# Kernel tuning notes

Hardware: AMD Instinct MI355X
Metric: run time of the kernel (lower is better)

The kernel has to match this reference:

```python
import jax, jax.numpy as jnp
import numpy as np

D_MODEL = 768
KAN_HIDDEN = 2048
NUM_CP = 16        # number of B-spline control points / coefficients per edge
DEGREE = 3         # cubic splines
RMIN, RMAX = -4.0, 4.0


def bspline_basis(x, num_cp=NUM_CP, degree=DEGREE, rmin=RMIN, rmax=RMAX):
    """Cox-de Boor B-spline basis.
    x: (N, D) -> basis: (N, D, num_cp). Uniform knots extended by `degree`
    on each side so that [rmin, rmax] has full basis support.
    """
    h = (rmax - rmin) / (num_cp - degree)
    # K = num_cp + degree + 1 knots
    knots = rmin - degree * h + jnp.arange(num_cp + degree + 1, dtype=x.dtype) * h
    xe = x[..., None]  # (N, D, 1)
    # degree-0 indicator bases: (N, D, num_cp + degree)
    b = ((xe >= knots[:-1]) & (xe < knots[1:])).astype(x.dtype)
    for d in range(1, degree + 1):
        t0 = knots[:-(d + 1)]   # t[k]
        t1 = knots[d:-1]        # t[k+d]
        t2 = knots[d + 1:]      # t[k+d+1]
        t3 = knots[1:-d]        # t[k+1]
        b = (xe - t0) / (t1 - t0) * b[..., :-1] + (t2 - xe) / (t2 - t3) * b[..., 1:]
    return b  # (N, D, num_cp)


def kan_layer(x, w):
    """x: (N, Din); w: (Dout, Din, num_cp) per-edge spline coefficients."""
    basis = bspline_basis(x)                      # (N, Din, K)
    return jnp.einsum('ndk,odk->no', basis, w)    # (N, Dout)


def setup_inputs() -> dict:
    key = jax.random.key(0)
    kx, k1, k2 = jax.random.split(key, 3)
    x = jax.random.normal(kx, (2, 2048, D_MODEL), dtype=jnp.float32)
    # spline coefficient tables, small init like nn.init scaled normal
    w1 = jax.random.normal(k1, (KAN_HIDDEN, D_MODEL, NUM_CP), dtype=jnp.float32) * (1.0 / np.sqrt(D_MODEL * NUM_CP))
    w2 = jax.random.normal(k2, (D_MODEL, KAN_HIDDEN, NUM_CP), dtype=jnp.float32) * (1.0 / np.sqrt(KAN_HIDDEN * NUM_CP))
    return {"x": x, "w1": w1, "w2": w2}


def reference(x, w1, w2):
    B, T, D = x.shape
    input_dtype = x.dtype
    h = x.reshape(B * T, D).astype(jnp.float32)
    h = kan_layer(h, w1)                # (B*T, KAN_HIDDEN)
    h = kan_layer(h, w2)                # (B*T, D_MODEL)
    h = h.astype(input_dtype)
    # dropout p=0.0 / eval mode -> identity
    return h.reshape(B, T, -1)
```

## Files before the change

### kernel.cpp

```cpp
#include <hip/hip_runtime.h>
#include <hip/hip_bf16.h>
#include <stdint.h>

typedef __attribute__((ext_vector_type(8))) short short8;
typedef __attribute__((ext_vector_type(4))) float f32x4;
typedef __attribute__((ext_vector_type(4))) int i32x4;

#define DMODEL 768
#define HID    2048
#define MROWS  4096

#define KINVH  (13.0f/8.0f)
#define KNOT0  (-4.0f - 3.0f*(8.0f/13.0f))

__device__ __forceinline__ unsigned short f2bf(float f) {
  __hip_bfloat16 h = __float2bfloat16(f);
  return *reinterpret_cast<unsigned short*>(&h);
}

template<int DIN>
__device__ __forceinline__ void pack_wave(const float* __restrict__ src,
                                          unsigned short* __restrict__ dst, int gw) {
  constexpr int NK2 = DIN / 2;
  int l   = threadIdx.x & 63;
  int cb  = gw / NK2;
  int kt2 = gw % NK2;
  int c16 = l & 15, q = l >> 4;
  int col = cb * 16 + c16;
  const float* s = src + ((size_t)col * DIN + kt2 * 2 + (q >> 1)) * 16 + (q & 1) * 8;
  float4 v0 = *(const float4*)s;
  float4 v1 = *(const float4*)(s + 4);
  short8 o;
  o[0] = (short)f2bf(v0.x); o[1] = (short)f2bf(v0.y);
  o[2] = (short)f2bf(v0.z); o[3] = (short)f2bf(v0.w);
  o[4] = (short)f2bf(v1.x); o[5] = (short)f2bf(v1.y);
  o[6] = (short)f2bf(v1.z); o[7] = (short)f2bf(v1.w);
  *(short8*)(dst + (((size_t)cb * NK2 + kt2) * 64 + q * 16 + c16) * 8) = o;
}

__global__ void __launch_bounds__(256) conv_pack1(const float* __restrict__ src,
                                                  unsigned short* __restrict__ dst) {
  pack_wave<DMODEL>(src, dst, blockIdx.x * 4 + (threadIdx.x >> 6));
}

__global__ void __launch_bounds__(256) pack2_reduce2(const float* __restrict__ w2,
                                                     unsigned short* __restrict__ dst,
                                                     float4* __restrict__ p, int n4) {
  constexpr int PACK_BLOCKS = ((DMODEL / 16) * (HID / 2)) / 4;
  int b = blockIdx.x;
  if (b < PACK_BLOCKS) {
    pack_wave<HID>(w2, dst, b * 4 + (threadIdx.x >> 6));
  } else {
    int i = (b - PACK_BLOCKS) * 256 + threadIdx.x;
    if (i < n4) {
      float4 a = p[i], q = p[i + n4];
      float4 r;
      r.x = a.x + q.x; r.y = a.y + q.y; r.z = a.z + q.z; r.w = a.w + q.w;
      p[i] = r;
    }
  }
}

__global__ void __launch_bounds__(256) reduce4(const float4* __restrict__ p,
                                               float4* __restrict__ out, int n4) {
  int i = blockIdx.x * 256 + threadIdx.x;
  if (i >= n4) return;
  float4 a = p[i], b = p[i + n4], c = p[i + 2 * n4], d = p[i + 3 * n4];
  float4 r;
  r.x = a.x + b.x + c.x + d.x;
  r.y = a.y + b.y + c.y + d.y;
  r.z = a.z + b.z + c.z + d.z;
  r.w = a.w + b.w + c.w + d.w;
  out[i] = r;
}

template<int DIN, int DOUT, int SPLITK>
__global__ void __launch_bounds__(256, 4)
kan_gemm(const float* __restrict__ X, const unsigned short* __restrict__ Wb,
         float* __restrict__ Out) {
  constexpr int BM  = 64;
  constexpr int BN  = 256;
  constexpr int NK  = (DIN * 16) / 64;
  constexpr int NK2 = DIN / 2;
  constexpr int NKS = NK / SPLITK;
  constexpr int GX  = MROWS / BM;
  constexpr int GY  = DOUT / BN;
  constexpr int CPX = (GX * GY) / 8;
  __shared__ __align__(16) char smA[BM * 128];

  const int tid  = threadIdx.x;
  const int lane = tid & 63;
  const int wid  = tid >> 6;

  const int d    = blockIdx.x + blockIdx.y * GX;
  const int lf   = (d & 7) * CPX + (d >> 3);
  const int brow = (lf % GX) * BM;
  const int bcol = (lf / GX) * BN;
  const int kt0  = blockIdx.z * NKS;
  const int kt1  = kt0 + NKS;

  f32x4 acc[4][4];
#pragma unroll
  for (int m = 0; m < 4; ++m)
#pragma unroll
    for (int n = 0; n < 4; ++n) acc[m][n] = (f32x4){0.f, 0.f, 0.f, 0.f};

  int a_base[4], a_sw[4];
#pragma unroll
  for (int m = 0; m < 4; ++m) {
    int row   = m * 16 + (lane & 15);
    a_base[m] = row * 128 + ((lane >> 4) * 16);
    a_sw[m]   = (row & 7) << 4;
  }

  const unsigned short* bp[4];
#pragma unroll
  for (int n = 0; n < 4; ++n)
    bp[n] = Wb + ((size_t)(bcol / 16 + wid * 4 + n) * NK2 + (size_t)kt0 * 2) * 512
               + lane * 8;

  const int br_ = tid >> 2;
  const int bd_ = tid & 3;
  const float* xrow = X + (size_t)(brow + br_) * DIN + bd_;

  float xcur = xrow[(size_t)kt0 * 4];
  short8 bv[2][4];
#pragma unroll
  for (int n = 0; n < 4; ++n) {
    bv[0][n] = *(const short8*)(bp[n]);
    bv[1][n] = *(const short8*)(bp[n] + 512);
    bp[n] += 1024;
  }

  for (int kt = kt0; kt < kt1; ++kt) {
    __syncthreads();

    {
      float u  = (xcur - KNOT0) * KINVH;
      float uf = floorf(u);
      int   jj = (int)uf;
      float t  = u - uf;
      float s1 = 1.0f - t;
      float t2 = t * t, t3 = t2 * t;
      float s2 = s1 * s1, s3 = s2 * s1;
      float p0 = s3 * (1.0f / 6.0f);
      float p3 = t3 * (1.0f / 6.0f);
      float p1 = fmaf(0.5f, t3, 2.0f / 3.0f) - t2;
      float p2 = fmaf(0.5f, s3, 2.0f / 3.0f) - s2;

      int base = br_ * 128 + bd_ * 32;
      int sw   = (br_ & 7) << 4;
      *(i32x4*)(smA + (base ^ sw))        = (i32x4){0, 0, 0, 0};
      *(i32x4*)(smA + ((base + 16) ^ sw)) = (i32x4){0, 0, 0, 0};
      unsigned short q0 = f2bf(p0), q1 = f2bf(p1), q2 = f2bf(p2), q3 = f2bf(p3);
      int k0 = jj - 3;
      if ((unsigned)(k0 + 0) < 16u) *(unsigned short*)(smA + ((base + (k0 + 0) * 2) ^ sw)) = q0;
      if ((unsigned)(k0 + 1) < 16u) *(unsigned short*)(smA + ((base + (k0 + 1) * 2) ^ sw)) = q1;
      if ((unsigned)(k0 + 2) < 16u) *(unsigned short*)(smA + ((base + (k0 + 2) * 2) ^ sw)) = q2;
      if ((unsigned)(k0 + 3) < 16u) *(unsigned short*)(smA + ((base + (k0 + 3) * 2) ^ sw)) = q3;
    }

    {
      int ktn = (kt + 1 < kt1) ? kt + 1 : kt;
      xcur = xrow[(size_t)ktn * 4];
    }

    __syncthreads();

#pragma unroll
    for (int kk = 0; kk < 2; ++kk) {
      short8 a[4];
#pragma unroll
      for (int m = 0; m < 4; ++m)
        a[m] = *(const short8*)(smA + ((a_base[m] + kk * 64) ^ a_sw[m]));
#pragma unroll
      for (int m = 0; m < 4; ++m)
#pragma unroll
        for (int n = 0; n < 4; ++n)
          acc[m][n] = __builtin_amdgcn_mfma_f32_16x16x32_bf16(a[m], bv[kk][n], acc[m][n], 0, 0, 0);
    }

    if (kt + 1 < kt1) {
#pragma unroll
      for (int n = 0; n < 4; ++n) {
        bv[0][n] = *(const short8*)(bp[n]);
        bv[1][n] = *(const short8*)(bp[n] + 512);
        bp[n] += 1024;
      }
    }
  }

  float* outp = Out + (size_t)blockIdx.z * MROWS * DOUT;
#pragma unroll
  for (int m = 0; m < 4; ++m)
#pragma unroll
    for (int n = 0; n < 4; ++n)
#pragma unroll
      for (int q = 0; q < 4; ++q) {
        int grow = brow + m * 16 + (lane >> 4) * 4 + q;
        int gcol = bcol + wid * 64 + n * 16 + (lane & 15);
        outp[(size_t)grow * DOUT + gcol] = acc[m][n][q];
      }
}

extern "C" void kernel_launch(void* const* d_in, const int* in_sizes, int n_in,
                              void* d_out, int out_size, void* d_ws, size_t ws_size,
                              hipStream_t stream) {
  const float* x  = (const float*)d_in[0];
  const float* w1 = (const float*)d_in[1];
  const float* w2 = (const float*)d_in[2];
  float* out = (float*)d_out;

  char* ws = (char*)d_ws;
  unsigned short* wgb   = (unsigned short*)ws;
  float*          part1 = (float*)(ws + 50331648);
  float*          hbf   = part1;
  float*          part2 = (float*)(ws + 83886080);

  conv_pack1<<<((HID / 16) * (DMODEL / 2)) / 4, 256, 0, stream>>>(w1, wgb);
  kan_gemm<DMODEL, HID, 2>
      <<<dim3(MROWS / 64, HID / 256, 2), 256, 0, stream>>>(x, wgb, part1);

  {
    const int hn4 = (MROWS * HID) / 4;
    const int packB = ((DMODEL / 16) * (HID / 2)) / 4;
    const int redB  = hn4 / 256;
    pack2_reduce2<<<packB + redB, 256, 0, stream>>>(w2, wgb, (float4*)part1, hn4);
  }
  kan_gemm<HID, DMODEL, 4>
      <<<dim3(MROWS / 64, DMODEL / 256, 4), 256, 0, stream>>>(hbf, wgb, part2);
  const int rn4 = (MROWS * DMODEL) / 4;
  reduce4<<<rn4 / 256, 256, 0, stream>>>((const float4*)part2, (float4*)out, rn4);
}
```

Before: 443.9 us.

## Warp-specialize KAN GEMM into basis-producer and MFMA-consumer waves with double-buffered LDS

Doubles the block to 512 threads. Four producer waves evaluate the B-spline basis into one of two LDS buffers while four consumer waves run MFMAs on the other, with one barrier per K-step instead of two. The aim is to hide the basis computation and LDS writes behind the matrix math. In exchange, each block uses more threads and twice the LDS, which may lower occupancy (launch_bounds 512,4), and producer waves sit idle during the epilogue.

```diff
diff --git a/kernel.cpp b/kernel.cpp
--- a/kernel.cpp
+++ b/kernel.cpp
@@ -12,6 +12,10 @@
 
 #define KINVH  (13.0f/8.0f)
 #define KNOT0  (-4.0f - 3.0f*(8.0f/13.0f))
+
+#define BAR_LDS() do { asm volatile("s_waitcnt lgkmcnt(0)" ::: "memory"); \
+                       __builtin_amdgcn_s_barrier(); \
+                       __builtin_amdgcn_sched_barrier(0); } while (0)
 
 __device__ __forceinline__ unsigned short f2bf(float f) {
   __hip_bfloat16 h = __float2bfloat16(f);
@@ -75,7 +79,7 @@
 }
 
 template<int DIN, int DOUT, int SPLITK>
-__global__ void __launch_bounds__(256, 4)
+__global__ void __launch_bounds__(512, 4)
 kan_gemm(const float* __restrict__ X, const unsigned short* __restrict__ Wb,
          float* __restrict__ Out) {
   constexpr int BM  = 64;
@@ -83,14 +87,17 @@
   constexpr int NK  = (DIN * 16) / 64;
   constexpr int NK2 = DIN / 2;
   constexpr int NKS = NK / SPLITK;
+  static_assert(NKS % 2 == 0, "even K-steps for buffer parity");
   constexpr int GX  = MROWS / BM;
   constexpr int GY  = DOUT / BN;
   constexpr int CPX = (GX * GY) / 8;
-  __shared__ __align__(16) char smA[BM * 128];
+  __shared__ __align__(16) char smA[2][BM * 128];
 
   const int tid  = threadIdx.x;
   const int lane = tid & 63;
   const int wid  = tid >> 6;
+  const bool prod = (wid >= 4);
+  const int cwid = wid & 3;
 
   const int d    = blockIdx.x + blockIdx.y * GX;
   const int lf   = (d & 7) * CPX + (d >> 3);
@@ -112,84 +119,96 @@
     a_base[m] = row * 128 + ((lane >> 4) * 16);
     a_sw[m]   = (row & 7) << 4;
   }
-
   const unsigned short* bp[4];
 #pragma unroll
   for (int n = 0; n < 4; ++n)
-    bp[n] = Wb + ((size_t)(bcol / 16 + wid * 4 + n) * NK2 + (size_t)kt0 * 2) * 512
+    bp[n] = Wb + ((size_t)(bcol / 16 + cwid * 4 + n) * NK2 + (size_t)kt0 * 2) * 512
                + lane * 8;
-
-  const int br_ = tid >> 2;
-  const int bd_ = tid & 3;
+  short8 bv[2][4];
+
+  const int pt  = tid & 255;
+  const int br_ = pt >> 2;
+  const int bd_ = pt & 3;
   const float* xrow = X + (size_t)(brow + br_) * DIN + bd_;
-
-  float xcur = xrow[(size_t)kt0 * 4];
-  short8 bv[2][4];
-#pragma unroll
-  for (int n = 0; n < 4; ++n) {
-    bv[0][n] = *(const short8*)(bp[n]);
-    bv[1][n] = *(const short8*)(bp[n] + 512);
-    bp[n] += 1024;
-  }
-
-  for (int kt = kt0; kt < kt1; ++kt) {
-    __syncthreads();
-
-    {
-      float u  = (xcur - KNOT0) * KINVH;
-      float uf = floorf(u);
-      int   jj = (int)uf;
-      float t  = u - uf;
-      float s1 = 1.0f - t;
-      float t2 = t * t, t3 = t2 * t;
-      float s2 = s1 * s1, s3 = s2 * s1;
-      float p0 = s3 * (1.0f / 6.0f);
-      float p3 = t3 * (1.0f / 6.0f);
-      float p1 = fmaf(0.5f, t3, 2.0f / 3.0f) - t2;
-      float p2 = fmaf(0.5f, s3, 2.0f / 3.0f) - s2;
-
-      int base = br_ * 128 + bd_ * 32;
-      int sw   = (br_ & 7) << 4;
-      *(i32x4*)(smA + (base ^ sw))        = (i32x4){0, 0, 0, 0};
-      *(i32x4*)(smA + ((base + 16) ^ sw)) = (i32x4){0, 0, 0, 0};
-      unsigned short q0 = f2bf(p0), q1 = f2bf(p1), q2 = f2bf(p2), q3 = f2bf(p3);
-      int k0 = jj - 3;
-      if ((unsigned)(k0 + 0) < 16u) *(unsigned short*)(smA + ((base + (k0 + 0) * 2) ^ sw)) = q0;
-      if ((unsigned)(k0 + 1) < 16u) *(unsigned short*)(smA + ((base + (k0 + 1) * 2) ^ sw)) = q1;
-      if ((unsigned)(k0 + 2) < 16u) *(unsigned short*)(smA + ((base + (k0 + 2) * 2) ^ sw)) = q2;
-      if ((unsigned)(k0 + 3) < 16u) *(unsigned short*)(smA + ((base + (k0 + 3) * 2) ^ sw)) = q3;
+  float xv = 0.f;
+
+  auto BASIS = [&](float x_, char* smp) {
+    float u  = (x_ - KNOT0) * KINVH;
+    float uf = floorf(u);
+    int   jj = (int)uf;
+    float t  = u - uf;
+    float s1 = 1.0f - t;
+    float t2 = t * t, t3 = t2 * t;
+    float s2 = s1 * s1, s3 = s2 * s1;
+    float p0 = s3 * (1.0f / 6.0f);
+    float p3 = t3 * (1.0f / 6.0f);
+    float p1 = fmaf(0.5f, t3, 2.0f / 3.0f) - t2;
+    float p2 = fmaf(0.5f, s3, 2.0f / 3.0f) - s2;
+
+    int base = br_ * 128 + bd_ * 32;
+    int sw   = (br_ & 7) << 4;
+    *(i32x4*)(smp + (base ^ sw))        = (i32x4){0, 0, 0, 0};
+    *(i32x4*)(smp + ((base + 16) ^ sw)) = (i32x4){0, 0, 0, 0};
+    unsigned short q0 = f2bf(p0), q1 = f2bf(p1), q2 = f2bf(p2), q3 = f2bf(p3);
+    int k0 = jj - 3;
+    if ((unsigned)(k0 + 0) < 16u) *(unsigned short*)(smp + ((base + (k0 + 0) * 2) ^ sw)) = q0;
+    if ((unsigned)(k0 + 1) < 16u) *(unsigned short*)(smp + ((base + (k0 + 1) * 2) ^ sw)) = q1;
+    if ((unsigned)(k0 + 2) < 16u) *(unsigned short*)(smp + ((base + (k0 + 2) * 2) ^ sw)) = q2;
+    if ((unsigned)(k0 + 3) < 16u) *(unsigned short*)(smp + ((base + (k0 + 3) * 2) ^ sw)) = q3;
+  };
+
+  if (!prod) {
+#pragma unroll
+    for (int n = 0; n < 4; ++n) {
+      bv[0][n] = *(const short8*)(bp[n]);
+      bv[1][n] = *(const short8*)(bp[n] + 512);
+      bp[n] += 1024;
     }
-
-    {
-      int ktn = (kt + 1 < kt1) ? kt + 1 : kt;
-      xcur = xrow[(size_t)ktn * 4];
+  } else {
+    BASIS(xrow[(size_t)kt0 * 4], &smA[0][0]);
+    xv = xrow[(size_t)(kt0 + 1) * 4];
+  }
+  BAR_LDS();
+
+  auto STEP = [&](int kt, char* smR, char* smW) {
+    const bool more = (kt + 1 < kt1);
+    if (!prod) {
+#pragma unroll
+      for (int kk = 0; kk < 2; ++kk) {
+        short8 a[4];
+#pragma unroll
+        for (int m = 0; m < 4; ++m)
+          a[m] = *(const short8*)(smR + ((a_base[m] + kk * 64) ^ a_sw[m]));
+#pragma unroll
+        for (int m = 0; m < 4; ++m)
+#pragma unroll
+          for (int n = 0; n < 4; ++n)
+            acc[m][n] = __builtin_amdgcn_mfma_f32_16x16x32_bf16(a[m], bv[kk][n], acc[m][n], 0, 0, 0);
+      }
+      if (more) {
+#pragma unroll
+        for (int n = 0; n < 4; ++n) {
+          bv[0][n] = *(const short8*)(bp[n]);
+          bv[1][n] = *(const short8*)(bp[n] + 512);
+          bp[n] += 1024;
+        }
+      }
+    } else {
+      if (more) {
+        BASIS(xv, smW);
+        int ktn = (kt + 2 < kt1) ? kt + 2 : kt1 - 1;
+        xv = xrow[(size_t)ktn * 4];
+      }
     }
-
-    __syncthreads();
-
-#pragma unroll
-    for (int kk = 0; kk < 2; ++kk) {
-      short8 a[4];
-#pragma unroll
-      for (int m = 0; m < 4; ++m)
-        a[m] = *(const short8*)(smA + ((a_base[m] + kk * 64) ^ a_sw[m]));
-#pragma unroll
-      for (int m = 0; m < 4; ++m)
-#pragma unroll
-        for (int n = 0; n < 4; ++n)
-          acc[m][n] = __builtin_amdgcn_mfma_f32_16x16x32_bf16(a[m], bv[kk][n], acc[m][n], 0, 0, 0);
-    }
-
-    if (kt + 1 < kt1) {
-#pragma unroll
-      for (int n = 0; n < 4; ++n) {
-        bv[0][n] = *(const short8*)(bp[n]);
-        bv[1][n] = *(const short8*)(bp[n] + 512);
-        bp[n] += 1024;
-      }
-    }
-  }
-
+    BAR_LDS();
+  };
+
+  for (int kt = kt0; kt < kt1; kt += 2) {
+    STEP(kt,     &smA[0][0], &smA[1][0]);
+    STEP(kt + 1, &smA[1][0], &smA[0][0]);
+  }
+
+  if (prod) return;
   float* outp = Out + (size_t)blockIdx.z * MROWS * DOUT;
 #pragma unroll
   for (int m = 0; m < 4; ++m)
@@ -198,7 +217,7 @@
 #pragma unroll
       for (int q = 0; q < 4; ++q) {
         int grow = brow + m * 16 + (lane >> 4) * 4 + q;
-        int gcol = bcol + wid * 64 + n * 16 + (lane & 15);
+        int gcol = bcol + cwid * 64 + n * 16 + (lane & 15);
         outp[(size_t)grow * DOUT + gcol] = acc[m][n][q];
       }
 }
@@ -219,7 +238,7 @@
 
   conv_pack1<<<((HID / 16) * (DMODEL / 2)) / 4, 256, 0, stream>>>(w1, wgb);
   kan_gemm<DMODEL, HID, 2>
-      <<<dim3(MROWS / 64, HID / 256, 2), 256, 0, stream>>>(x, wgb, part1);
+      <<<dim3(MROWS / 64, HID / 256, 2), 512, 0, stream>>>(x, wgb, part1);
 
   {
     const int hn4 = (MROWS * HID) / 4;
@@ -228,7 +247,7 @@
     pack2_reduce2<<<packB + redB, 256, 0, stream>>>(w2, wgb, (float4*)part1, hn4);
   }
   kan_gemm<HID, DMODEL, 4>
-      <<<dim3(MROWS / 64, DMODEL / 256, 4), 256, 0, stream>>>(hbf, wgb, part2);
+      <<<dim3(MROWS / 64, DMODEL / 256, 4), 512, 0, stream>>>(hbf, wgb, part2);
   const int rn4 = (MROWS * DMODEL) / 4;
   reduce4<<<rn4 / 256, 256, 0, stream>>>((const float4*)part2, (float4*)out, rn4);
 }
```

Measured after the change: 459.2 us. 3.4% more time.
